# Performance work log

Measured on AMD Instinct MI355X. Metric: run time of the kernel, lower is better.

The kernel has to match this reference:

```python
import jax, jax.numpy as jnp
import numpy as np

N = 65536      # total nodes (64 graphs x 1024 nodes)
E = 1048576    # total edges
B = 64         # graphs in the batch
H = 128        # in_dim == hidden_dim
HEAD = 4
EPS = 1e-5


def setup_inputs() -> dict:
    key = jax.random.key(0)
    ks = jax.random.split(key, 16)
    s = 0.02
    return {
        "h": jax.random.normal(ks[0], (N, H), jnp.float32),
        "inter_f": jax.random.normal(ks[1], (B, H), jnp.float32),
        "gamma1": jnp.ones((H,), jnp.float32), "beta1": jnp.zeros((H,), jnp.float32),
        "W1": jax.random.normal(ks[2], (H, H), jnp.float32) * s, "b1": jnp.zeros((H,), jnp.float32),
        "gamma2": jnp.ones((H,), jnp.float32), "beta2": jnp.zeros((H,), jnp.float32),
        "W2": jax.random.normal(ks[3], (H, H), jnp.float32) * s, "b2": jnp.zeros((H,), jnp.float32),
        "Wq": jax.random.normal(ks[4], (HEAD, H, H), jnp.float32) * s,
        "Wk": jax.random.normal(ks[5], (HEAD, H, H), jnp.float32) * s,
        "Wv": jax.random.normal(ks[6], (HEAD, H, H), jnp.float32) * s,
        "Wc": jax.random.normal(ks[7], (HEAD * H, H), jnp.float32) * s,
        "ln_g": jnp.ones((H,), jnp.float32), "ln_b": jnp.zeros((H,), jnp.float32),
        "Wf1": jax.random.normal(ks[8], (H, 2 * H), jnp.float32) * s, "bf1": jnp.zeros((2 * H,), jnp.float32),
        "Wf2": jax.random.normal(ks[9], (2 * H, H), jnp.float32) * s, "bf2": jnp.zeros((H,), jnp.float32),
        "src": jax.random.randint(ks[10], (E,), 0, N, jnp.int32),
        "dst": jax.random.randint(ks[11], (E,), 0, N, jnp.int32),
        "graph_id": (jnp.arange(N) // (N // B)).astype(jnp.int32),
    }


def _bn(x, g, b):
    # BatchNorm1d (training-mode batch statistics, biased var)
    m = x.mean(0)
    v = jnp.mean((x - m) ** 2, 0)
    return (x - m) * jax.lax.rsqrt(v + EPS) * g + b


def _ln(x, g, b):
    m = x.mean(-1, keepdims=True)
    v = jnp.mean((x - m) ** 2, -1, keepdims=True)
    return (x - m) * jax.lax.rsqrt(v + EPS) * g + b


def _gconv(x, W, b, src, dst):
    # dgl GraphConv, norm='both': D_out^{-1/2} gather -> scatter-add -> D_in^{-1/2}, then W, b
    ones_e = jnp.ones((E,), x.dtype)
    dout = jnp.maximum(jax.ops.segment_sum(ones_e, src, num_segments=N), 1.0)
    din = jnp.maximum(jax.ops.segment_sum(ones_e, dst, num_segments=N), 1.0)
    msg = (x * jax.lax.rsqrt(dout)[:, None])[src]            # [E, H] gather
    agg = jax.ops.segment_sum(msg, dst, num_segments=N)      # [N, H] scatter-add
    agg = agg * jax.lax.rsqrt(din)[:, None]
    return agg @ W + b


def _forward(h, inter_f, gamma1, beta1, W1, b1, gamma2, beta2, W2, b2,
             Wq, Wk, Wv, Wc, ln_g, ln_b, Wf1, bf1, Wf2, bf2, src, dst, graph_id):
    # init pooling (mean_nodes)
    counts = jax.ops.segment_sum(jnp.ones((N,), h.dtype), graph_id, num_segments=B)
    init_avg_h = jax.ops.segment_sum(h, graph_id, num_segments=B) / counts[:, None]

    # two residual GraphConv blocks (dropout is identity at inference)
    h1 = h + jax.nn.relu(_gconv(_bn(h, gamma1, beta1), W1, b1, src, dst))
    h2 = h1 + jax.nn.relu(_gconv(_bn(h1, gamma2, beta2), W2, b2, src, dst))

    # broadcast_nodes(inter_f)
    inter_h = inter_f[graph_id]                               # [N, H]

    # transformer_block: per-head q/k/v, per-node scalar att, per-graph segment softmax
    q = jnp.einsum('nd,hdo->hno', h2, Wq)
    k = jnp.einsum('nd,hdo->hno', inter_h, Wk)
    v = jnp.einsum('nd,hdo->hno', h2, Wv)
    att = jnp.sum(q * k, axis=-1) / jnp.sqrt(jnp.float32(1280.0))   # [HEAD, N]
    mx = jax.vmap(lambda a: jax.ops.segment_max(a, graph_id, num_segments=B))(att)  # [HEAD, B]
    e = jnp.exp(att - mx[:, graph_id])
    ssum = jax.vmap(lambda a: jax.ops.segment_sum(a, graph_id, num_segments=B))(e)
    alpha = e / ssum[:, graph_id]                             # segment softmax per head
    tp = v * alpha[..., None]                                 # [HEAD, N, H]
    mo = tp.transpose(1, 0, 2).reshape(N, HEAD * H) @ Wc      # concat heads + project

    x1 = _ln(mo + h2, ln_g, ln_b)
    x2 = _ln(jax.nn.relu(x1 @ Wf1 + bf1) @ Wf2 + bf2 + x1, ln_g, ln_b)

    readout = jax.ops.segment_sum(x2, graph_id, num_segments=B)     # sum_nodes
    return readout, init_avg_h


def reference(h, inter_f, gamma1, beta1, W1, b1, gamma2, beta2, W2, b2,
              Wq, Wk, Wv, Wc, ln_g, ln_b, Wf1, bf1, Wf2, bf2, src, dst, graph_id):
    return _forward(h, inter_f, gamma1, beta1, W1, b1, gamma2, beta2, W2, b2,
                    Wq, Wk, Wv, Wc, ln_g, ln_b, Wf1, bf1, Wf2, bf2, src, dst, graph_id)
```

## Files before the change

kernel.cpp:

```cpp
#include <hip/hip_runtime.h>

#define NN 65536
#define NE 1048576
#define NB 64
#define HD 128
#define HD2 256
#define NHEAD 4
#define NPG 1024
#define BEPS 1e-5f
#define BM 64
#define ESTRIDE 20480

typedef short bf16x8s __attribute__((ext_vector_type(8)));
typedef float f32x4 __attribute__((ext_vector_type(4)));
#define MFMA16(a,b,c) __builtin_amdgcn_mfma_f32_16x16x32_bf16(a,b,c,0,0,0)

__device__ __forceinline__ unsigned short f2bf(float f) {
    union { float f; unsigned int u; } x{f};
    unsigned int r = x.u + 0x7FFFu + ((x.u >> 16) & 1u);
    return (unsigned short)(r >> 16);
}
__device__ __forceinline__ float b2f(unsigned short s) {
    union { unsigned int u; float f; } x{((unsigned int)s) << 16};
    return x.f;
}
__device__ __forceinline__ void atomAddF(float* p, float v) { unsafeAtomicAdd(p, v); }

__global__ __launch_bounds__(256) void k_prep_pool(const int* __restrict__ src, const int* __restrict__ dst,
                                                   int* __restrict__ gcurD, int* __restrict__ gcurS,
                                                   unsigned int* __restrict__ dbuck, unsigned short* __restrict__ sbuck,
                                                   const float* __restrict__ h, float* __restrict__ out_avg,
                                                   float* __restrict__ colsum, float* __restrict__ colsq) {
    __shared__ int cntD[64], cntS[64], baseD[64], baseS[64];
    __shared__ float ls[256], lq[256];
    const int t = threadIdx.x;
    if (blockIdx.x < 512) {
        if (t < 64) { cntD[t] = 0; cntS[t] = 0; }
        __syncthreads();
        const int e0 = blockIdx.x * 2048;
        int sv[8], dv[8];
        #pragma unroll
        for (int j = 0; j < 8; ++j) {
            int e = e0 + j * 256 + t;
            sv[j] = src[e]; dv[j] = dst[e];
            atomicAdd(&cntD[dv[j] >> 10], 1);
            atomicAdd(&cntS[sv[j] >> 10], 1);
        }
        __syncthreads();
        if (t < 64) baseD[t] = atomicAdd(&gcurD[t], cntD[t]);
        else if (t < 128) baseS[t - 64] = atomicAdd(&gcurS[t - 64], cntS[t - 64]);
        __syncthreads();
        if (t < 64) { cntD[t] = 0; cntS[t] = 0; }
        __syncthreads();
        #pragma unroll
        for (int j = 0; j < 8; ++j) {
            int gd = dv[j] >> 10;
            int slot = baseD[gd] + atomicAdd(&cntD[gd], 1);
            if (slot < ESTRIDE)
                dbuck[gd * ESTRIDE + slot] = (unsigned)(dv[j] & 1023) | ((unsigned)sv[j] << 10);
            int gs = sv[j] >> 10;
            int slot2 = baseS[gs] + atomicAdd(&cntS[gs], 1);
            if (slot2 < ESTRIDE)
                sbuck[gs * ESTRIDE + slot2] = (unsigned short)(sv[j] & 1023);
        }
    } else {
        int b2 = blockIdx.x - 512;
        int r0 = b2 * 64;
        int c = t & 127, half = t >> 7;
        float s = 0.f, sq = 0.f;
        for (int r = r0 + half * 32; r < r0 + half * 32 + 32; ++r) {
            float v = h[(size_t)r * HD + c];
            s += v; sq += v * v;
        }
        ls[t] = s; lq[t] = sq;
        __syncthreads();
        if (t < 128) {
            s = ls[t] + ls[t + 128]; sq = lq[t] + lq[t + 128];
            atomAddF(&out_avg[(r0 >> 10) * HD + t], s * (1.0f / NPG));
            atomAddF(&colsum[t], s);
            atomAddF(&colsq[t], sq);
        }
    }
}

__global__ __launch_bounds__(1024) void k_prep2(const int* __restrict__ gcurD, const int* __restrict__ gcurS,
                                                const unsigned int* __restrict__ dbuck,
                                                const unsigned short* __restrict__ sbuck,
                                                float* __restrict__ din_r, float* __restrict__ dout_r,
                                                int* __restrict__ beg, int* __restrict__ endv,
                                                int* __restrict__ elist) {
    __shared__ int hist[1024];
    __shared__ int pre[1024];
    const int t = threadIdx.x;
    const int b = blockIdx.x;
    if (b < 64) {
        const int g = b;
        const int n = min(gcurD[g], ESTRIDE);
        const unsigned int* pd = dbuck + g * ESTRIDE;
        hist[t] = 0;
        __syncthreads();
        for (int i = t; i < n; i += 1024) atomicAdd(&hist[pd[i] & 1023], 1);
        __syncthreads();
        const int cnt = hist[t];
        din_r[g * 1024 + t] = rsqrtf((float)max(cnt, 1));
        int x = cnt; pre[t] = x;
        __syncthreads();
        #pragma unroll
        for (int off = 1; off < 1024; off <<= 1) {
            int v = (t >= off) ? pre[t - off] : 0;
            __syncthreads();
            x += v; pre[t] = x;
            __syncthreads();
        }
        const int excl = x - cnt;
        beg[g * 1024 + t]  = g * ESTRIDE + excl;
        endv[g * 1024 + t] = g * ESTRIDE + excl + cnt;
        __syncthreads();
        hist[t] = excl; pre[t] = 0;
        __syncthreads();
        for (int i = t; i < n; i += 1024) {
            unsigned int w = pd[i];
            int dl = w & 1023;
            int r = atomicAdd(&pre[dl], 1);
            elist[g * ESTRIDE + hist[dl] + r] = (int)(w >> 10);
        }
    } else {
        const int g = b - 64;
        const int m = min(gcurS[g], ESTRIDE);
        const unsigned short* ps = sbuck + g * ESTRIDE;
        hist[t] = 0;
        __syncthreads();
        for (int i = t; i < m; i += 1024) atomicAdd(&hist[ps[i]], 1);
        __syncthreads();
        dout_r[g * 1024 + t] = rsqrtf((float)max(hist[t], 1));
    }
}

__device__ __forceinline__ void dev_prepW(int idx, const float* __restrict__ W,
                                          unsigned short* __restrict__ frag, int O) {
    int l = idx & 63, tt = idx >> 6;
    int ot = O >> 4;
    int c = tt % ot, ks = tt / ot;
    int q = l >> 4, m = l & 15;
    const float* wp = W + (size_t)(ks * 32 + q * 8) * O + c * 16 + m;
    union { uint4 v; unsigned short u[8]; } pk;
    #pragma unroll
    for (int j = 0; j < 8; ++j) pk.u[j] = f2bf(wp[(size_t)j * O]);
    *(uint4*)(frag + (size_t)idx * 8) = pk.v;
}

__global__ __launch_bounds__(256) void k_wprep(const float* __restrict__ W1, const float* __restrict__ W2,
                                               const float* __restrict__ Wf1, const float* __restrict__ Wf2,
                                               const float* __restrict__ interf, const float* __restrict__ Wk,
                                               const float* __restrict__ Wq, const float* __restrict__ Wv,
                                               const float* __restrict__ Wc,
                                               unsigned short* __restrict__ W1f, unsigned short* __restrict__ W2f,
                                               unsigned short* __restrict__ Wf1f, unsigned short* __restrict__ Wf2f,
                                               float* __restrict__ watt, unsigned short* __restrict__ Uf) {
    const int b = blockIdx.x, t = threadIdx.x;
    if (b < 8)        dev_prepW(b * 256 + t, W1, W1f, 128);
    else if (b < 16)  dev_prepW((b - 8) * 256 + t, W2, W2f, 128);
    else if (b < 32)  dev_prepW((b - 16) * 256 + t, Wf1, Wf1f, 256);
    else if (b < 48)  dev_prepW((b - 32) * 256 + t, Wf2, Wf2f, 128);
    else if (b < 304) {
        int hb = b - 48;
        int hh = hb >> 6, g = hb & 63;
        __shared__ float f[HD];
        __shared__ float kv[HD];
        if (t < HD) f[t] = interf[g * HD + t];
        __syncthreads();
        if (t < HD) {
            const float* Wkh = Wk + (size_t)hh * HD * HD;
            float s = 0.f;
            for (int d = 0; d < HD; ++d) s += f[d] * Wkh[(size_t)d * HD + t];
            kv[t] = s;
        }
        __syncthreads();
        if (t < HD) {
            const float* row = Wq + ((size_t)hh * HD + t) * HD;
            float s2 = 0.f;
            #pragma unroll 4
            for (int o = 0; o < HD; o += 4) {
                float4 w = *(const float4*)(row + o);
                s2 += w.x * kv[o] + w.y * kv[o + 1] + w.z * kv[o + 2] + w.w * kv[o + 3];
            }
            watt[hb * HD + t] = s2 * 0.027950849718747373f;
        }
    } else {
        int idx = (b - 304) * 256 + t;
        int o = idx & 127;
        int d = (idx >> 7) & 127;
        int hh = idx >> 14;
        const float* wv = Wv + ((size_t)hh * HD + d) * HD;
        const float* wc = Wc + (size_t)(hh * HD) * HD + o;
        float s = 0.f;
        for (int m2 = 0; m2 < HD; ++m2) s += wv[m2] * wc[(size_t)m2 * HD];
        int ks = d >> 5, dd = d & 31, q = dd >> 3, j = dd & 7;
        int c = o >> 4, m = o & 15, l = q * 16 + m;
        Uf[(size_t)((((hh * 4 + ks) * 8 + c) * 64 + l) * 8 + j)] = f2bf(s);
    }
}

__global__ __launch_bounds__(256) void k_bnpack(const float* __restrict__ x,
                                                const float* __restrict__ colsum, const float* __restrict__ colsq,
                                                const float* __restrict__ gma, const float* __restrict__ bta,
                                                const float* __restrict__ dout_r, unsigned short* __restrict__ xn) {
    int idx = blockIdx.x * 256 + threadIdx.x;
    int node = idx >> 4;
    int c8 = (idx & 15) * 8;
    float sc[8], sh[8];
    #pragma unroll
    for (int j = 0; j < 8; ++j) {
        float mean = colsum[c8 + j] * (1.0f / NN);
        float var  = colsq[c8 + j] * (1.0f / NN) - mean * mean;
        float rstd = rsqrtf(var + BEPS);
        sc[j] = rstd * gma[c8 + j];
        sh[j] = bta[c8 + j] - mean * sc[j];
    }
    float dr = dout_r[node];
    float4 v0 = *(const float4*)(x + (size_t)node * HD + c8);
    float4 v1 = *(const float4*)(x + (size_t)node * HD + c8 + 4);
    union { uint4 v; unsigned short u[8]; } pk;
    pk.u[0] = f2bf((v0.x * sc[0] + sh[0]) * dr);
    pk.u[1] = f2bf((v0.y * sc[1] + sh[1]) * dr);
    pk.u[2] = f2bf((v0.z * sc[2] + sh[2]) * dr);
    pk.u[3] = f2bf((v0.w * sc[3] + sh[3]) * dr);
    pk.u[4] = f2bf((v1.x * sc[4] + sh[4]) * dr);
    pk.u[5] = f2bf((v1.y * sc[5] + sh[5]) * dr);
    pk.u[6] = f2bf((v1.z * sc[6] + sh[6]) * dr);
    pk.u[7] = f2bf((v1.w * sc[7] + sh[7]) * dr);
    *(uint4*)(xn + (size_t)node * HD + c8) = pk.v;
}

__global__ __launch_bounds__(256) void k_aggregate(const unsigned short* __restrict__ xn,
                                                   const float* __restrict__ din_r,
                                                   const int* __restrict__ beg, const int* __restrict__ endv,
                                                   const int* __restrict__ elist,
                                                   unsigned short* __restrict__ agg) {
    const int tid = threadIdx.x;
    const int node = blockIdx.x * 4 + (tid >> 6);
    const int c2 = (tid & 63) * 2;
    const int b0 = beg[node], e0 = endv[node];
    float a0 = 0.f, a1 = 0.f;
    int i = b0;
    for (; i + 4 <= e0; i += 4) {
        int s0 = elist[i], s1 = elist[i + 1], s2 = elist[i + 2], s3 = elist[i + 3];
        unsigned int v0 = *(const unsigned int*)(xn + (size_t)s0 * HD + c2);
        unsigned int v1 = *(const unsigned int*)(xn + (size_t)s1 * HD + c2);
        unsigned int v2 = *(const unsigned int*)(xn + (size_t)s2 * HD + c2);
        unsigned int v3 = *(const unsigned int*)(xn + (size_t)s3 * HD + c2);
        a0 += b2f((unsigned short)v0) + b2f((unsigned short)v1) + b2f((unsigned short)v2) + b2f((unsigned short)v3);
        a1 += b2f((unsigned short)(v0 >> 16)) + b2f((unsigned short)(v1 >> 16))
            + b2f((unsigned short)(v2 >> 16)) + b2f((unsigned short)(v3 >> 16));
    }
    for (; i < e0; ++i) {
        int s = elist[i];
        unsigned int v = *(const unsigned int*)(xn + (size_t)s * HD + c2);
        a0 += b2f((unsigned short)v);
        a1 += b2f((unsigned short)(v >> 16));
    }
    float dn = din_r[node];
    ushort2 o;
    o.x = f2bf(a0 * dn); o.y = f2bf(a1 * dn);
    *(ushort2*)(agg + (size_t)node * HD + c2) = o;
}

template<bool SCORES, bool STATS>
__global__ __launch_bounds__(256) void k_gconv_mfma(const unsigned short* __restrict__ agg,
                                                    const unsigned short* __restrict__ Wfrag,
                                                    const float* __restrict__ bias,
                                                    const float* __restrict__ res, float* __restrict__ outp,
                                                    const float* __restrict__ watt, float* __restrict__ att,
                                                    float* __restrict__ colsum, float* __restrict__ colsq) {
    __shared__ float credS[4 * HD];
    __shared__ float credQ[4 * HD];
    const int tid = threadIdx.x;
    const int w = tid >> 6, l = tid & 63, q = l >> 4, m = l & 15;
    const int node = blockIdx.x * BM + w * 16 + m;
    bf16x8s a[4];
    #pragma unroll
    for (int ks = 0; ks < 4; ++ks)
        a[ks] = *(const bf16x8s*)(agg + (size_t)node * HD + ks * 32 + q * 8);
    f32x4 acc[8] = {};
    #pragma unroll
    for (int ks = 0; ks < 4; ++ks) {
        #pragma unroll
        for (int c = 0; c < 8; ++c) {
            bf16x8s b = *(const bf16x8s*)(Wfrag + (size_t)((ks * 8 + c) * 64 + l) * 8);
            acc[c] = MFMA16(b, a[ks], acc[c]);
        }
    }
    float vals[8][4];
    #pragma unroll
    for (int c = 0; c < 8; ++c) {
        const int col = c * 16 + q * 4;
        float4 bv = *(const float4*)(bias + col);
        float4 rv = *(const float4*)(res + (size_t)node * HD + col);
        vals[c][0] = rv.x + fmaxf(acc[c][0] + bv.x, 0.f);
        vals[c][1] = rv.y + fmaxf(acc[c][1] + bv.y, 0.f);
        vals[c][2] = rv.z + fmaxf(acc[c][2] + bv.z, 0.f);
        vals[c][3] = rv.w + fmaxf(acc[c][3] + bv.w, 0.f);
        *(float4*)(outp + (size_t)node * HD + col) = make_float4(vals[c][0], vals[c][1], vals[c][2], vals[c][3]);
    }
    if (SCORES) {
        const int g = node >> 10;
        #pragma unroll
        for (int hh = 0; hh < NHEAD; ++hh) {
            const float* wp = watt + ((size_t)(hh * NB + g)) * HD;
            float s = 0.f;
            #pragma unroll
            for (int c = 0; c < 8; ++c) {
                const int col = c * 16 + q * 4;
                float4 wv = *(const float4*)(wp + col);
                s += vals[c][0] * wv.x + vals[c][1] * wv.y + vals[c][2] * wv.z + vals[c][3] * wv.w;
            }
            s += __shfl_xor(s, 16, 64);
            s += __shfl_xor(s, 32, 64);
            if (q == 0) att[(size_t)hh * NN + node] = s;
        }
    }
    if (STATS) {
        #pragma unroll
        for (int c = 0; c < 8; ++c) {
            #pragma unroll
            for (int r = 0; r < 4; ++r) {
                float v = vals[c][r];
                float vq = v * v;
                #pragma unroll
                for (int mk = 1; mk <= 8; mk <<= 1) {
                    v  += __shfl_xor(v, mk, 64);
                    vq += __shfl_xor(vq, mk, 64);
                }
                if (m == 0) {
                    credS[w * HD + c * 16 + q * 4 + r] = v;
                    credQ[w * HD + c * 16 + q * 4 + r] = vq;
                }
            }
        }
        __syncthreads();
        if (tid < HD) {
            float s = credS[tid] + credS[HD + tid] + credS[2 * HD + tid] + credS[3 * HD + tid];
            float sq = credQ[tid] + credQ[HD + tid] + credQ[2 * HD + tid] + credQ[3 * HD + tid];
            atomAddF(&colsum[tid], s);
            atomAddF(&colsq[tid], sq);
        }
    }
}

__global__ __launch_bounds__(256) void k_segsoftmax(const float* __restrict__ att, float* __restrict__ alpha) {
    const int hh = blockIdx.x >> 6, g = blockIdx.x & 63;
    const int t = threadIdx.x;
    const float* a = att + (size_t)hh * NN + g * NPG;
    float* al = alpha + (size_t)hh * NN + g * NPG;
    float v[4]; float mx = -1e30f;
    #pragma unroll
    for (int i = 0; i < 4; ++i) { v[i] = a[t + i * 256]; mx = fmaxf(mx, v[i]); }
    #pragma unroll
    for (int m = 32; m > 0; m >>= 1) mx = fmaxf(mx, __shfl_xor(mx, m, 64));
    __shared__ float redm[4], reds[4];
    if ((t & 63) == 0) redm[t >> 6] = mx;
    __syncthreads();
    mx = fmaxf(fmaxf(redm[0], redm[1]), fmaxf(redm[2], redm[3]));
    float s = 0.f;
    #pragma unroll
    for (int i = 0; i < 4; ++i) { v[i] = __expf(v[i] - mx); s += v[i]; }
    #pragma unroll
    for (int m = 32; m > 0; m >>= 1) s += __shfl_xor(s, m, 64);
    if ((t & 63) == 0) reds[t >> 6] = s;
    __syncthreads();
    s = reds[0] + reds[1] + reds[2] + reds[3];
    float inv = 1.f / s;
    #pragma unroll
    for (int i = 0; i < 4; ++i) al[t + i * 256] = v[i] * inv;
}

__global__ __launch_bounds__(256) void k_mo_x1(const float* __restrict__ h2,
                                               const unsigned short* __restrict__ Ufrag,
                                               const float* __restrict__ alpha,
                                               const float* __restrict__ lng, const float* __restrict__ lnb,
                                               float* __restrict__ x1) {
    const int tid = threadIdx.x;
    const int w = tid >> 6, l = tid & 63, q = l >> 4, m = l & 15;
    const int node = blockIdx.x * BM + w * 16 + m;
    bf16x8s a[4];
    #pragma unroll
    for (int ks = 0; ks < 4; ++ks) {
        float4 v0 = *(const float4*)(h2 + (size_t)node * HD + ks * 32 + q * 8);
        float4 v1 = *(const float4*)(h2 + (size_t)node * HD + ks * 32 + q * 8 + 4);
        union { bf16x8s v; unsigned short u[8]; } pk;
        pk.u[0] = f2bf(v0.x); pk.u[1] = f2bf(v0.y); pk.u[2] = f2bf(v0.z); pk.u[3] = f2bf(v0.w);
        pk.u[4] = f2bf(v1.x); pk.u[5] = f2bf(v1.y); pk.u[6] = f2bf(v1.z); pk.u[7] = f2bf(v1.w);
        a[ks] = pk.v;
    }
    f32x4 mo[8] = {};
    #pragma unroll
    for (int hh = 0; hh < 4; ++hh) {
        f32x4 acc[8] = {};
        #pragma unroll
        for (int ks = 0; ks < 4; ++ks) {
            #pragma unroll
            for (int c = 0; c < 8; ++c) {
                bf16x8s b = *(const bf16x8s*)(Ufrag + (size_t)(((hh * 4 + ks) * 8 + c) * 64 + l) * 8);
                acc[c] = MFMA16(b, a[ks], acc[c]);
            }
        }
        float al = alpha[(size_t)hh * NN + node];
        #pragma unroll
        for (int c = 0; c < 8; ++c) {
            mo[c][0] += al * acc[c][0];
            mo[c][1] += al * acc[c][1];
            mo[c][2] += al * acc[c][2];
            mo[c][3] += al * acc[c][3];
        }
    }
    float vals[8][4]; float s = 0.f, sq = 0.f;
    #pragma unroll
    for (int c = 0; c < 8; ++c) {
        const int col = c * 16 + q * 4;
        float4 hv = *(const float4*)(h2 + (size_t)node * HD + col);
        vals[c][0] = mo[c][0] + hv.x;
        vals[c][1] = mo[c][1] + hv.y;
        vals[c][2] = mo[c][2] + hv.z;
        vals[c][3] = mo[c][3] + hv.w;
        #pragma unroll
        for (int r = 0; r < 4; ++r) { s += vals[c][r]; sq += vals[c][r] * vals[c][r]; }
    }
    s  += __shfl_xor(s, 16, 64);  s  += __shfl_xor(s, 32, 64);
    sq += __shfl_xor(sq, 16, 64); sq += __shfl_xor(sq, 32, 64);
    float mean = s * (1.f / HD);
    float var  = sq * (1.f / HD) - mean * mean;
    float rstd = rsqrtf(var + BEPS);
    #pragma unroll
    for (int c = 0; c < 8; ++c) {
        const int col = c * 16 + q * 4;
        float4 gv = *(const float4*)(lng + col);
        float4 bv = *(const float4*)(lnb + col);
        float4 o;
        o.x = (vals[c][0] - mean) * rstd * gv.x + bv.x;
        o.y = (vals[c][1] - mean) * rstd * gv.y + bv.y;
        o.z = (vals[c][2] - mean) * rstd * gv.z + bv.z;
        o.w = (vals[c][3] - mean) * rstd * gv.w + bv.w;
        *(float4*)(x1 + (size_t)node * HD + col) = o;
    }
}

__global__ __launch_bounds__(256) void k_ffn1_mfma(const float* __restrict__ X,
                                                   const unsigned short* __restrict__ Wfrag,
                                                   const float* __restrict__ bias,
                                                   unsigned short* __restrict__ mid) {
    const int tid = threadIdx.x;
    const int w = tid >> 6, l = tid & 63, q = l >> 4, m = l & 15;
    const int node = blockIdx.x * BM + w * 16 + m;
    bf16x8s a[4];
    #pragma unroll
    for (int ks = 0; ks < 4; ++ks) {
        float4 v0 = *(const float4*)(X + (size_t)node * HD + ks * 32 + q * 8);
        float4 v1 = *(const float4*)(X + (size_t)node * HD + ks * 32 + q * 8 + 4);
        union { bf16x8s v; unsigned short u[8]; } pk;
        pk.u[0] = f2bf(v0.x); pk.u[1] = f2bf(v0.y); pk.u[2] = f2bf(v0.z); pk.u[3] = f2bf(v0.w);
        pk.u[4] = f2bf(v1.x); pk.u[5] = f2bf(v1.y); pk.u[6] = f2bf(v1.z); pk.u[7] = f2bf(v1.w);
        a[ks] = pk.v;
    }
    f32x4 acc[16] = {};
    #pragma unroll
    for (int ks = 0; ks < 4; ++ks) {
        #pragma unroll
        for (int c = 0; c < 16; ++c) {
            bf16x8s b = *(const bf16x8s*)(Wfrag + (size_t)((ks * 16 + c) * 64 + l) * 8);
            acc[c] = MFMA16(b, a[ks], acc[c]);
        }
    }
    #pragma unroll
    for (int c = 0; c < 16; ++c) {
        const int col = c * 16 + q * 4;
        float4 bv = *(const float4*)(bias + col);
        ushort4 o;
        o.x = f2bf(fmaxf(acc[c][0] + bv.x, 0.f));
        o.y = f2bf(fmaxf(acc[c][1] + bv.y, 0.f));
        o.z = f2bf(fmaxf(acc[c][2] + bv.z, 0.f));
        o.w = f2bf(fmaxf(acc[c][3] + bv.w, 0.f));
        *(ushort4*)(mid + (size_t)node * HD2 + col) = o;
    }
}

__global__ __launch_bounds__(256) void k_ffn2_mfma(const unsigned short* __restrict__ mid,
                                                   const unsigned short* __restrict__ Wfrag,
                                                   const float* __restrict__ bias,
                                                   const float* __restrict__ x1,
                                                   const float* __restrict__ lng, const float* __restrict__ lnb,
                                                   float* __restrict__ outp) {
    __shared__ float cred[4 * HD];
    const int tid = threadIdx.x;
    const int w = tid >> 6, l = tid & 63, q = l >> 4, m = l & 15;
    const int node = blockIdx.x * BM + w * 16 + m;
    bf16x8s a[8];
    #pragma unroll
    for (int ks = 0; ks < 8; ++ks)
        a[ks] = *(const bf16x8s*)(mid + (size_t)node * HD2 + ks * 32 + q * 8);
    f32x4 acc[8] = {};
    #pragma unroll
    for (int ks = 0; ks < 8; ++ks) {
        #pragma unroll
        for (int c = 0; c < 8; ++c) {
            bf16x8s b = *(const bf16x8s*)(Wfrag + (size_t)((ks * 8 + c) * 64 + l) * 8);
            acc[c] = MFMA16(b, a[ks], acc[c]);
        }
    }
    float vals[8][4]; float s = 0.f, sq = 0.f;
    #pragma unroll
    for (int c = 0; c < 8; ++c) {
        const int col = c * 16 + q * 4;
        float4 bv = *(const float4*)(bias + col);
        float4 xv = *(const float4*)(x1 + (size_t)node * HD + col);
        vals[c][0] = acc[c][0] + bv.x + xv.x;
        vals[c][1] = acc[c][1] + bv.y + xv.y;
        vals[c][2] = acc[c][2] + bv.z + xv.z;
        vals[c][3] = acc[c][3] + bv.w + xv.w;
        #pragma unroll
        for (int r = 0; r < 4; ++r) { s += vals[c][r]; sq += vals[c][r] * vals[c][r]; }
    }
    s  += __shfl_xor(s, 16, 64);  s  += __shfl_xor(s, 32, 64);
    sq += __shfl_xor(sq, 16, 64); sq += __shfl_xor(sq, 32, 64);
    float mean = s * (1.f / HD);
    float var  = sq * (1.f / HD) - mean * mean;
    float rstd = rsqrtf(var + BEPS);
    #pragma unroll
    for (int c = 0; c < 8; ++c) {
        const int col = c * 16 + q * 4;
        float4 gv = *(const float4*)(lng + col);
        float4 bv = *(const float4*)(lnb + col);
        float4 o;
        o.x = (vals[c][0] - mean) * rstd * gv.x + bv.x;
        o.y = (vals[c][1] - mean) * rstd * gv.y + bv.y;
        o.z = (vals[c][2] - mean) * rstd * gv.z + bv.z;
        o.w = (vals[c][3] - mean) * rstd * gv.w + bv.w;
        #pragma unroll
        for (int mk = 1; mk <= 8; mk <<= 1) {
            o.x += __shfl_xor(o.x, mk, 64);
            o.y += __shfl_xor(o.y, mk, 64);
            o.z += __shfl_xor(o.z, mk, 64);
            o.w += __shfl_xor(o.w, mk, 64);
        }
        if (m == 0) *(float4*)(cred + w * HD + col) = o;
    }
    __syncthreads();
    if (tid < HD) {
        float sum = cred[tid] + cred[HD + tid] + cred[2 * HD + tid] + cred[3 * HD + tid];
        int g = blockIdx.x >> 4;
        atomAddF(&outp[g * HD + tid], sum);
    }
}

extern "C" void kernel_launch(void* const* d_in, const int* in_sizes, int n_in,
                              void* d_out, int out_size, void* d_ws, size_t ws_size,
                              hipStream_t stream) {
    (void)in_sizes; (void)n_in; (void)out_size;
    const float* h      = (const float*)d_in[0];
    const float* interf = (const float*)d_in[1];
    const float* gamma1 = (const float*)d_in[2];
    const float* beta1  = (const float*)d_in[3];
    const float* W1     = (const float*)d_in[4];
    const float* b1     = (const float*)d_in[5];
    const float* gamma2 = (const float*)d_in[6];
    const float* beta2  = (const float*)d_in[7];
    const float* W2     = (const float*)d_in[8];
    const float* b2     = (const float*)d_in[9];
    const float* Wq     = (const float*)d_in[10];
    const float* Wk     = (const float*)d_in[11];
    const float* Wv     = (const float*)d_in[12];
    const float* Wc     = (const float*)d_in[13];
    const float* ln_g   = (const float*)d_in[14];
    const float* ln_b   = (const float*)d_in[15];
    const float* Wf1    = (const float*)d_in[16];
    const float* bf1    = (const float*)d_in[17];
    const float* Wf2    = (const float*)d_in[18];
    const float* bf2    = (const float*)d_in[19];
    const int*   src    = (const int*)d_in[20];
    const int*   dst    = (const int*)d_in[21];

    float* out = (float*)d_out;
    float* R1 = (float*)d_ws;
    float* R2 = R1 + 8388608;
    float* R3 = R2 + 8388608;
    float* aux = R3 + 8388608;

    float* h1 = R1;
    float* x1 = R1;
    unsigned int*   dbuck = (unsigned int*)R1;
    unsigned short* sbuck = (unsigned short*)(R1 + 1310720);
    float* h2 = R2;
    int*   elist = (int*)R2;
    unsigned short* mid  = (unsigned short*)R2;
    unsigned short* xn   = (unsigned short*)R3;
    unsigned short* aggb = (unsigned short*)(R3 + 4194304);
    float* att   = R3;
    float* alpha = R3 + 262144;

    float* dout_r  = aux;
    float* din_r   = aux + 65536;
    float* colsum1 = aux + 131072;
    float* colsq1  = aux + 131200;
    float* colsum2 = aux + 131328;
    float* colsq2  = aux + 131456;
    int*   gcurD   = (int*)(aux + 131584);
    int*   gcurS   = (int*)(aux + 131648);
    float* watt    = aux + 131712;
    int*   beg     = (int*)(aux + 164480);
    int*   endv    = (int*)(aux + 230016);
    unsigned short* W1f  = (unsigned short*)(aux + 295552);
    unsigned short* W2f  = (unsigned short*)(aux + 303744);
    unsigned short* Wf1f = (unsigned short*)(aux + 311936);
    unsigned short* Wf2f = (unsigned short*)(aux + 328320);
    unsigned short* Uf   = (unsigned short*)(aux + 344704);

    if (ws_size < (size_t)(25165824 + 377472) * 4) return;

    hipMemsetAsync(out, 0, 16384 * 4, stream);
    hipMemsetAsync(colsum1, 0, 640 * 4, stream);

    k_prep_pool<<<1536, 256, 0, stream>>>(src, dst, gcurD, gcurS, dbuck, sbuck,
                                          h, out + 8192, colsum1, colsq1);
    k_prep2<<<128, 1024, 0, stream>>>(gcurD, gcurS, dbuck, sbuck, din_r, dout_r, beg, endv, elist);
    k_wprep<<<560, 256, 0, stream>>>(W1, W2, Wf1, Wf2, interf, Wk, Wq, Wv, Wc,
                                     W1f, W2f, Wf1f, Wf2f, watt, Uf);

    k_bnpack<<<4096, 256, 0, stream>>>(h, colsum1, colsq1, gamma1, beta1, dout_r, xn);
    k_aggregate<<<16384, 256, 0, stream>>>(xn, din_r, beg, endv, elist, aggb);
    k_gconv_mfma<false, true><<<1024, 256, 0, stream>>>(aggb, W1f, b1, h, h1, nullptr, nullptr, colsum2, colsq2);

    k_bnpack<<<4096, 256, 0, stream>>>(h1, colsum2, colsq2, gamma2, beta2, dout_r, xn);
    k_aggregate<<<16384, 256, 0, stream>>>(xn, din_r, beg, endv, elist, aggb);
    k_gconv_mfma<true, false><<<1024, 256, 0, stream>>>(aggb, W2f, b2, h1, h2, watt, att, nullptr, nullptr);

    k_segsoftmax<<<256, 256, 0, stream>>>(att, alpha);
    k_mo_x1<<<1024, 256, 0, stream>>>(h2, Uf, alpha, ln_g, ln_b, x1);

    k_ffn1_mfma<<<1024, 256, 0, stream>>>(x1, Wf1f, bf1, mid);
    k_ffn2_mfma<<<1024, 256, 0, stream>>>(mid, Wf2f, bf2, x1, ln_g, ln_b, out);
}
```

Before: 339.6 us.

## Fuse attention, FFN and readout into one kernel; bf16 intermediates; deterministic reductions

Merges the multi-head attention projection, the first LayerNorm, both FFN matmuls and the second LayerNorm into one kernel that keeps x1 and the FFN hidden activations in shared memory instead of round-tripping them through global memory. The h1 and h2 intermediates are now stored as bf16 instead of fp32, which halves their traffic but adds rounding error to residuals and BN statistics. Float atomics for column statistics and the readout are replaced by per-block partial buffers plus small reduction kernels, and the edge-bucketing kernel moves to larger blocks with padded global counters. These steps add kernel launches and change numerical precision in exchange for less memory traffic and less atomic contention.

```diff
diff --git a/kernel.cpp b/kernel.cpp
--- a/kernel.cpp
+++ b/kernel.cpp
@@ -24,36 +24,34 @@
     union { unsigned int u; float f; } x{((unsigned int)s) << 16};
     return x.f;
 }
-__device__ __forceinline__ void atomAddF(float* p, float v) { unsafeAtomicAdd(p, v); }
-
-__global__ __launch_bounds__(256) void k_prep_pool(const int* __restrict__ src, const int* __restrict__ dst,
-                                                   int* __restrict__ gcurD, int* __restrict__ gcurS,
-                                                   unsigned int* __restrict__ dbuck, unsigned short* __restrict__ sbuck,
-                                                   const float* __restrict__ h, float* __restrict__ out_avg,
-                                                   float* __restrict__ colsum, float* __restrict__ colsq) {
-    __shared__ int cntD[64], cntS[64], baseD[64], baseS[64];
-    __shared__ float ls[256], lq[256];
+
+__global__ __launch_bounds__(1024) void k_prep_pool(const int* __restrict__ src, const int* __restrict__ dst,
+                                                    int* __restrict__ gcurD, int* __restrict__ gcurS,
+                                                    unsigned int* __restrict__ dbuck, unsigned short* __restrict__ sbuck,
+                                                    const float* __restrict__ h,
+                                                    float* __restrict__ psum, float* __restrict__ psq) {
     const int t = threadIdx.x;
-    if (blockIdx.x < 512) {
+    if (blockIdx.x < 64) {
+        __shared__ int cntD[64], cntS[64], baseD[64], baseS[64];
         if (t < 64) { cntD[t] = 0; cntS[t] = 0; }
         __syncthreads();
-        const int e0 = blockIdx.x * 2048;
-        int sv[8], dv[8];
-        #pragma unroll
-        for (int j = 0; j < 8; ++j) {
-            int e = e0 + j * 256 + t;
+        const int e0 = blockIdx.x * 16384;
+        int sv[16], dv[16];
+        #pragma unroll
+        for (int j = 0; j < 16; ++j) {
+            int e = e0 + j * 1024 + t;
             sv[j] = src[e]; dv[j] = dst[e];
             atomicAdd(&cntD[dv[j] >> 10], 1);
             atomicAdd(&cntS[sv[j] >> 10], 1);
         }
         __syncthreads();
-        if (t < 64) baseD[t] = atomicAdd(&gcurD[t], cntD[t]);
-        else if (t < 128) baseS[t - 64] = atomicAdd(&gcurS[t - 64], cntS[t - 64]);
+        if (t < 64) baseD[t] = atomicAdd(&gcurD[t * 32], cntD[t]);
+        else if (t < 128) baseS[t - 64] = atomicAdd(&gcurS[(t - 64) * 32], cntS[t - 64]);
         __syncthreads();
         if (t < 64) { cntD[t] = 0; cntS[t] = 0; }
         __syncthreads();
         #pragma unroll
-        for (int j = 0; j < 8; ++j) {
+        for (int j = 0; j < 16; ++j) {
             int gd = dv[j] >> 10;
             int slot = baseD[gd] + atomicAdd(&cntD[gd], 1);
             if (slot < ESTRIDE)
@@ -64,21 +62,23 @@
                 sbuck[gs * ESTRIDE + slot2] = (unsigned short)(sv[j] & 1023);
         }
     } else {
-        int b2 = blockIdx.x - 512;
-        int r0 = b2 * 64;
-        int c = t & 127, half = t >> 7;
+        __shared__ float ls[1024], lq[1024];
+        const int bb = blockIdx.x - 64;
+        const int r0 = bb * 256;
+        const int c = t & 127, strip8 = t >> 7;
         float s = 0.f, sq = 0.f;
-        for (int r = r0 + half * 32; r < r0 + half * 32 + 32; ++r) {
-            float v = h[(size_t)r * HD + c];
+        for (int i = 0; i < 32; ++i) {
+            float v = h[(size_t)(r0 + strip8 * 32 + i) * HD + c];
             s += v; sq += v * v;
         }
         ls[t] = s; lq[t] = sq;
         __syncthreads();
         if (t < 128) {
-            s = ls[t] + ls[t + 128]; sq = lq[t] + lq[t + 128];
-            atomAddF(&out_avg[(r0 >> 10) * HD + t], s * (1.0f / NPG));
-            atomAddF(&colsum[t], s);
-            atomAddF(&colsq[t], sq);
+            float ss = 0.f, qq = 0.f;
+            #pragma unroll
+            for (int k = 0; k < 8; ++k) { ss += ls[t + k * 128]; qq += lq[t + k * 128]; }
+            psum[bb * HD + t] = ss;
+            psq[bb * HD + t]  = qq;
         }
     }
 }
@@ -95,7 +95,7 @@
     const int b = blockIdx.x;
     if (b < 64) {
         const int g = b;
-        const int n = min(gcurD[g], ESTRIDE);
+        const int n = min(gcurD[g * 32], ESTRIDE);
         const unsigned int* pd = dbuck + g * ESTRIDE;
         hist[t] = 0;
         __syncthreads();
@@ -126,7 +126,7 @@
         }
     } else {
         const int g = b - 64;
-        const int m = min(gcurS[g], ESTRIDE);
+        const int m = min(gcurS[g * 32], ESTRIDE);
         const unsigned short* ps = sbuck + g * ESTRIDE;
         hist[t] = 0;
         __syncthreads();
@@ -156,7 +156,10 @@
                                                const float* __restrict__ Wc,
                                                unsigned short* __restrict__ W1f, unsigned short* __restrict__ W2f,
                                                unsigned short* __restrict__ Wf1f, unsigned short* __restrict__ Wf2f,
-                                               float* __restrict__ watt, unsigned short* __restrict__ Uf) {
+                                               float* __restrict__ watt, unsigned short* __restrict__ Uf,
+                                               const float* __restrict__ psum, const float* __restrict__ psq,
+                                               float* __restrict__ out_avg,
+                                               float* __restrict__ colsum, float* __restrict__ colsq) {
     const int b = blockIdx.x, t = threadIdx.x;
     if (b < 8)        dev_prepW(b * 256 + t, W1, W1f, 128);
     else if (b < 16)  dev_prepW((b - 8) * 256 + t, W2, W2f, 128);
@@ -186,7 +189,7 @@
             }
             watt[hb * HD + t] = s2 * 0.027950849718747373f;
         }
-    } else {
+    } else if (b < 560) {
         int idx = (b - 304) * 256 + t;
         int o = idx & 127;
         int d = (idx >> 7) & 127;
@@ -198,10 +201,29 @@
         int ks = d >> 5, dd = d & 31, q = dd >> 3, j = dd & 7;
         int c = o >> 4, m = o & 15, l = q * 16 + m;
         Uf[(size_t)((((hh * 4 + ks) * 8 + c) * 64 + l) * 8 + j)] = f2bf(s);
-    }
-}
-
-__global__ __launch_bounds__(256) void k_bnpack(const float* __restrict__ x,
+    } else {
+        const int col = b - 560;
+        __shared__ float ls[256], lq[256];
+        ls[t] = psum[t * HD + col];
+        lq[t] = psq[t * HD + col];
+        __syncthreads();
+        if (t < 64) {
+            float a4 = ls[4 * t] + ls[4 * t + 1] + ls[4 * t + 2] + ls[4 * t + 3];
+            out_avg[t * HD + col] = a4 * (1.0f / NPG);
+            float b4 = lq[4 * t] + lq[4 * t + 1] + lq[4 * t + 2] + lq[4 * t + 3];
+            float ts = a4, tq = b4;
+            #pragma unroll
+            for (int mk = 1; mk <= 32; mk <<= 1) {
+                ts += __shfl_xor(ts, mk, 64);
+                tq += __shfl_xor(tq, mk, 64);
+            }
+            if (t == 0) { colsum[col] = ts; colsq[col] = tq; }
+        }
+    }
+}
+
+template<bool IN32>
+__global__ __launch_bounds__(256) void k_bnpack(const void* __restrict__ xin,
                                                 const float* __restrict__ colsum, const float* __restrict__ colsq,
                                                 const float* __restrict__ gma, const float* __restrict__ bta,
                                                 const float* __restrict__ dout_r, unsigned short* __restrict__ xn) {
@@ -218,17 +240,23 @@
         sh[j] = bta[c8 + j] - mean * sc[j];
     }
     float dr = dout_r[node];
-    float4 v0 = *(const float4*)(x + (size_t)node * HD + c8);
-    float4 v1 = *(const float4*)(x + (size_t)node * HD + c8 + 4);
+    float v[8];
+    if (IN32) {
+        const float* x = (const float*)xin;
+        float4 v0 = *(const float4*)(x + (size_t)node * HD + c8);
+        float4 v1 = *(const float4*)(x + (size_t)node * HD + c8 + 4);
+        v[0] = v0.x; v[1] = v0.y; v[2] = v0.z; v[3] = v0.w;
+        v[4] = v1.x; v[5] = v1.y; v[6] = v1.z; v[7] = v1.w;
+    } else {
+        const unsigned short* x = (const unsigned short*)xin;
+        union { uint4 u; unsigned short s[8]; } r;
+        r.u = *(const uint4*)(x + (size_t)node * HD + c8);
+        #pragma unroll
+        for (int j = 0; j < 8; ++j) v[j] = b2f(r.s[j]);
+    }
     union { uint4 v; unsigned short u[8]; } pk;
-    pk.u[0] = f2bf((v0.x * sc[0] + sh[0]) * dr);
-    pk.u[1] = f2bf((v0.y * sc[1] + sh[1]) * dr);
-    pk.u[2] = f2bf((v0.z * sc[2] + sh[2]) * dr);
-    pk.u[3] = f2bf((v0.w * sc[3] + sh[3]) * dr);
-    pk.u[4] = f2bf((v1.x * sc[4] + sh[4]) * dr);
-    pk.u[5] = f2bf((v1.y * sc[5] + sh[5]) * dr);
-    pk.u[6] = f2bf((v1.z * sc[6] + sh[6]) * dr);
-    pk.u[7] = f2bf((v1.w * sc[7] + sh[7]) * dr);
+    #pragma unroll
+    for (int j = 0; j < 8; ++j) pk.u[j] = f2bf((v[j] * sc[j] + sh[j]) * dr);
     *(uint4*)(xn + (size_t)node * HD + c8) = pk.v;
 }
 
@@ -265,13 +293,13 @@
     *(ushort2*)(agg + (size_t)node * HD + c2) = o;
 }
 
-template<bool SCORES, bool STATS>
+template<bool SCORES, bool STATS, bool RES32>
 __global__ __launch_bounds__(256) void k_gconv_mfma(const unsigned short* __restrict__ agg,
                                                     const unsigned short* __restrict__ Wfrag,
                                                     const float* __restrict__ bias,
-                                                    const float* __restrict__ res, float* __restrict__ outp,
+                                                    const void* __restrict__ res, unsigned short* __restrict__ outp,
                                                     const float* __restrict__ watt, float* __restrict__ att,
-                                                    float* __restrict__ colsum, float* __restrict__ colsq) {
+                                                    float* __restrict__ part2s, float* __restrict__ part2q) {
     __shared__ float credS[4 * HD];
     __shared__ float credQ[4 * HD];
     const int tid = threadIdx.x;
@@ -295,12 +323,22 @@
     for (int c = 0; c < 8; ++c) {
         const int col = c * 16 + q * 4;
         float4 bv = *(const float4*)(bias + col);
-        float4 rv = *(const float4*)(res + (size_t)node * HD + col);
-        vals[c][0] = rv.x + fmaxf(acc[c][0] + bv.x, 0.f);
-        vals[c][1] = rv.y + fmaxf(acc[c][1] + bv.y, 0.f);
-        vals[c][2] = rv.z + fmaxf(acc[c][2] + bv.z, 0.f);
-        vals[c][3] = rv.w + fmaxf(acc[c][3] + bv.w, 0.f);
-        *(float4*)(outp + (size_t)node * HD + col) = make_float4(vals[c][0], vals[c][1], vals[c][2], vals[c][3]);
+        float rv[4];
+        if (RES32) {
+            float4 r4 = *(const float4*)((const float*)res + (size_t)node * HD + col);
+            rv[0] = r4.x; rv[1] = r4.y; rv[2] = r4.z; rv[3] = r4.w;
+        } else {
+            ushort4 r4 = *(const ushort4*)((const unsigned short*)res + (size_t)node * HD + col);
+            rv[0] = b2f(r4.x); rv[1] = b2f(r4.y); rv[2] = b2f(r4.z); rv[3] = b2f(r4.w);
+        }
+        vals[c][0] = rv[0] + fmaxf(acc[c][0] + bv.x, 0.f);
+        vals[c][1] = rv[1] + fmaxf(acc[c][1] + bv.y, 0.f);
+        vals[c][2] = rv[2] + fmaxf(acc[c][2] + bv.z, 0.f);
+        vals[c][3] = rv[3] + fmaxf(acc[c][3] + bv.w, 0.f);
+        ushort4 o;
+        o.x = f2bf(vals[c][0]); o.y = f2bf(vals[c][1]);
+        o.z = f2bf(vals[c][2]); o.w = f2bf(vals[c][3]);
+        *(ushort4*)(outp + (size_t)node * HD + col) = o;
     }
     if (SCORES) {
         const int g = node >> 10;
@@ -339,12 +377,33 @@
         }
         __syncthreads();
         if (tid < HD) {
-            float s = credS[tid] + credS[HD + tid] + credS[2 * HD + tid] + credS[3 * HD + tid];
-            float sq = credQ[tid] + credQ[HD + tid] + credQ[2 * HD + tid] + credQ[3 * HD + tid];
-            atomAddF(&colsum[tid], s);
-            atomAddF(&colsq[tid], sq);
-        }
-    }
+            part2s[(size_t)blockIdx.x * HD + tid] =
+                credS[tid] + credS[HD + tid] + credS[2 * HD + tid] + credS[3 * HD + tid];
+            part2q[(size_t)blockIdx.x * HD + tid] =
+                credQ[tid] + credQ[HD + tid] + credQ[2 * HD + tid] + credQ[3 * HD + tid];
+        }
+    }
+}
+
+__global__ __launch_bounds__(256) void k_red2(const float* __restrict__ part2s, const float* __restrict__ part2q,
+                                              float* __restrict__ colsum, float* __restrict__ colsq) {
+    __shared__ float ws[8];
+    const int col = blockIdx.x, t = threadIdx.x;
+    float s = 0.f, sq = 0.f;
+    #pragma unroll
+    for (int k = 0; k < 4; ++k) {
+        s  += part2s[(size_t)(t + k * 256) * HD + col];
+        sq += part2q[(size_t)(t + k * 256) * HD + col];
+    }
+    #pragma unroll
+    for (int mk = 1; mk <= 32; mk <<= 1) {
+        s  += __shfl_xor(s, mk, 64);
+        sq += __shfl_xor(sq, mk, 64);
+    }
+    if ((t & 63) == 0) { ws[(t >> 6) * 2] = s; ws[(t >> 6) * 2 + 1] = sq; }
+    __syncthreads();
+    if (t == 0) colsum[col] = ws[0] + ws[2] + ws[4] + ws[6];
+    if (t == 1) colsq[col]  = ws[1] + ws[3] + ws[5] + ws[7];
 }
 
 __global__ __launch_bounds__(256) void k_segsoftmax(const float* __restrict__ att, float* __restrict__ alpha) {
@@ -374,24 +433,26 @@
     for (int i = 0; i < 4; ++i) al[t + i * 256] = v[i] * inv;
 }
 
-__global__ __launch_bounds__(256) void k_mo_x1(const float* __restrict__ h2,
-                                               const unsigned short* __restrict__ Ufrag,
-                                               const float* __restrict__ alpha,
-                                               const float* __restrict__ lng, const float* __restrict__ lnb,
-                                               float* __restrict__ x1) {
+__global__ __launch_bounds__(256) void k_mega(const unsigned short* __restrict__ h2b,
+                                              const unsigned short* __restrict__ Ufrag,
+                                              const float* __restrict__ alpha,
+                                              const float* __restrict__ lng, const float* __restrict__ lnb,
+                                              const unsigned short* __restrict__ Wf1f,
+                                              const unsigned short* __restrict__ Wf2f,
+                                              const float* __restrict__ bf1v, const float* __restrict__ bf2v,
+                                              float* __restrict__ rpart) {
+    __shared__ unsigned short x1l[64][136];
+    __shared__ unsigned short midl[64][264];
+    __shared__ float cred[4 * HD];
     const int tid = threadIdx.x;
     const int w = tid >> 6, l = tid & 63, q = l >> 4, m = l & 15;
     const int node = blockIdx.x * BM + w * 16 + m;
+    const int row = w * 16 + m;
+
     bf16x8s a[4];
     #pragma unroll
-    for (int ks = 0; ks < 4; ++ks) {
-        float4 v0 = *(const float4*)(h2 + (size_t)node * HD + ks * 32 + q * 8);
-        float4 v1 = *(const float4*)(h2 + (size_t)node * HD + ks * 32 + q * 8 + 4);
-        union { bf16x8s v; unsigned short u[8]; } pk;
-        pk.u[0] = f2bf(v0.x); pk.u[1] = f2bf(v0.y); pk.u[2] = f2bf(v0.z); pk.u[3] = f2bf(v0.w);
-        pk.u[4] = f2bf(v1.x); pk.u[5] = f2bf(v1.y); pk.u[6] = f2bf(v1.z); pk.u[7] = f2bf(v1.w);
-        a[ks] = pk.v;
-    }
+    for (int ks = 0; ks < 4; ++ks)
+        a[ks] = *(const bf16x8s*)(h2b + (size_t)node * HD + ks * 32 + q * 8);
     f32x4 mo[8] = {};
     #pragma unroll
     for (int hh = 0; hh < 4; ++hh) {
@@ -413,15 +474,90 @@
             mo[c][3] += al * acc[c][3];
         }
     }
+    {
+        float vals[8][4]; float s = 0.f, sq = 0.f;
+        #pragma unroll
+        for (int c = 0; c < 8; ++c) {
+            const int col = c * 16 + q * 4;
+            ushort4 hv = *(const ushort4*)(h2b + (size_t)node * HD + col);
+            vals[c][0] = mo[c][0] + b2f(hv.x);
+            vals[c][1] = mo[c][1] + b2f(hv.y);
+            vals[c][2] = mo[c][2] + b2f(hv.z);
+            vals[c][3] = mo[c][3] + b2f(hv.w);
+            #pragma unroll
+            for (int r = 0; r < 4; ++r) { s += vals[c][r]; sq += vals[c][r] * vals[c][r]; }
+        }
+        s  += __shfl_xor(s, 16, 64);  s  += __shfl_xor(s, 32, 64);
+        sq += __shfl_xor(sq, 16, 64); sq += __shfl_xor(sq, 32, 64);
+        float mean = s * (1.f / HD);
+        float var  = sq * (1.f / HD) - mean * mean;
+        float rstd = rsqrtf(var + BEPS);
+        #pragma unroll
+        for (int c = 0; c < 8; ++c) {
+            const int col = c * 16 + q * 4;
+            float4 gv = *(const float4*)(lng + col);
+            float4 bv = *(const float4*)(lnb + col);
+            ushort4 o;
+            o.x = f2bf((vals[c][0] - mean) * rstd * gv.x + bv.x);
+            o.y = f2bf((vals[c][1] - mean) * rstd * gv.y + bv.y);
+            o.z = f2bf((vals[c][2] - mean) * rstd * gv.z + bv.z);
+            o.w = f2bf((vals[c][3] - mean) * rstd * gv.w + bv.w);
+            *(ushort4*)(&x1l[row][col]) = o;
+        }
+    }
+    __syncthreads();
+
+    {
+        bf16x8s a2[4];
+        #pragma unroll
+        for (int ks = 0; ks < 4; ++ks)
+            a2[ks] = *(const bf16x8s*)(&x1l[row][ks * 32 + q * 8]);
+        f32x4 accB[16] = {};
+        #pragma unroll
+        for (int ks = 0; ks < 4; ++ks) {
+            #pragma unroll
+            for (int c = 0; c < 16; ++c) {
+                bf16x8s b = *(const bf16x8s*)(Wf1f + (size_t)((ks * 16 + c) * 64 + l) * 8);
+                accB[c] = MFMA16(b, a2[ks], accB[c]);
+            }
+        }
+        #pragma unroll
+        for (int c = 0; c < 16; ++c) {
+            const int col = c * 16 + q * 4;
+            float4 bv = *(const float4*)(bf1v + col);
+            ushort4 o;
+            o.x = f2bf(fmaxf(accB[c][0] + bv.x, 0.f));
+            o.y = f2bf(fmaxf(accB[c][1] + bv.y, 0.f));
+            o.z = f2bf(fmaxf(accB[c][2] + bv.z, 0.f));
+            o.w = f2bf(fmaxf(accB[c][3] + bv.w, 0.f));
+            *(ushort4*)(&midl[row][col]) = o;
+        }
+    }
+    __syncthreads();
+
+    bf16x8s a3[8];
+    #pragma unroll
+    for (int ks = 0; ks < 8; ++ks)
+        a3[ks] = *(const bf16x8s*)(&midl[row][ks * 32 + q * 8]);
+    f32x4 accC[8] = {};
+    #pragma unroll
+    for (int ks = 0; ks < 8; ++ks) {
+        #pragma unroll
+        for (int c = 0; c < 8; ++c) {
+            bf16x8s b = *(const bf16x8s*)(Wf2f + (size_t)((ks * 8 + c) * 64 + l) * 8);
+            accC[c] = MFMA16(b, a3[ks], accC[c]);
+        }
+    }
     float vals[8][4]; float s = 0.f, sq = 0.f;
     #pragma unroll
     for (int c = 0; c < 8; ++c) {
         const int col = c * 16 + q * 4;
-        float4 hv = *(const float4*)(h2 + (size_t)node * HD + col);
-        vals[c][0] = mo[c][0] + hv.x;
-        vals[c][1] = mo[c][1] + hv.y;
-        vals[c][2] = mo[c][2] + hv.z;
-        vals[c][3] = mo[c][3] + hv.w;
+        float4 bv = *(const float4*)(bf2v + col);
+        ushort4 xv = *(const ushort4*)(&x1l[row][col]);
+        vals[c][0] = accC[c][0] + bv.x + b2f(xv.x);
+        vals[c][1] = accC[c][1] + bv.y + b2f(xv.y);
+        vals[c][2] = accC[c][2] + bv.z + b2f(xv.z);
+        vals[c][3] = accC[c][3] + bv.w + b2f(xv.w);
         #pragma unroll
         for (int r = 0; r < 4; ++r) { s += vals[c][r]; sq += vals[c][r] * vals[c][r]; }
     }
@@ -440,100 +576,6 @@
         o.y = (vals[c][1] - mean) * rstd * gv.y + bv.y;
         o.z = (vals[c][2] - mean) * rstd * gv.z + bv.z;
         o.w = (vals[c][3] - mean) * rstd * gv.w + bv.w;
-        *(float4*)(x1 + (size_t)node * HD + col) = o;
-    }
-}
-
-__global__ __launch_bounds__(256) void k_ffn1_mfma(const float* __restrict__ X,
-                                                   const unsigned short* __restrict__ Wfrag,
-                                                   const float* __restrict__ bias,
-                                                   unsigned short* __restrict__ mid) {
-    const int tid = threadIdx.x;
-    const int w = tid >> 6, l = tid & 63, q = l >> 4, m = l & 15;
-    const int node = blockIdx.x * BM + w * 16 + m;
-    bf16x8s a[4];
-    #pragma unroll
-    for (int ks = 0; ks < 4; ++ks) {
-        float4 v0 = *(const float4*)(X + (size_t)node * HD + ks * 32 + q * 8);
-        float4 v1 = *(const float4*)(X + (size_t)node * HD + ks * 32 + q * 8 + 4);
-        union { bf16x8s v; unsigned short u[8]; } pk;
-        pk.u[0] = f2bf(v0.x); pk.u[1] = f2bf(v0.y); pk.u[2] = f2bf(v0.z); pk.u[3] = f2bf(v0.w);
-        pk.u[4] = f2bf(v1.x); pk.u[5] = f2bf(v1.y); pk.u[6] = f2bf(v1.z); pk.u[7] = f2bf(v1.w);
-        a[ks] = pk.v;
-    }
-    f32x4 acc[16] = {};
-    #pragma unroll
-    for (int ks = 0; ks < 4; ++ks) {
-        #pragma unroll
-        for (int c = 0; c < 16; ++c) {
-            bf16x8s b = *(const bf16x8s*)(Wfrag + (size_t)((ks * 16 + c) * 64 + l) * 8);
-            acc[c] = MFMA16(b, a[ks], acc[c]);
-        }
-    }
-    #pragma unroll
-    for (int c = 0; c < 16; ++c) {
-        const int col = c * 16 + q * 4;
-        float4 bv = *(const float4*)(bias + col);
-        ushort4 o;
-        o.x = f2bf(fmaxf(acc[c][0] + bv.x, 0.f));
-        o.y = f2bf(fmaxf(acc[c][1] + bv.y, 0.f));
-        o.z = f2bf(fmaxf(acc[c][2] + bv.z, 0.f));
-        o.w = f2bf(fmaxf(acc[c][3] + bv.w, 0.f));
-        *(ushort4*)(mid + (size_t)node * HD2 + col) = o;
-    }
-}
-
-__global__ __launch_bounds__(256) void k_ffn2_mfma(const unsigned short* __restrict__ mid,
-                                                   const unsigned short* __restrict__ Wfrag,
-                                                   const float* __restrict__ bias,
-                                                   const float* __restrict__ x1,
-                                                   const float* __restrict__ lng, const float* __restrict__ lnb,
-                                                   float* __restrict__ outp) {
-    __shared__ float cred[4 * HD];
-    const int tid = threadIdx.x;
-    const int w = tid >> 6, l = tid & 63, q = l >> 4, m = l & 15;
-    const int node = blockIdx.x * BM + w * 16 + m;
-    bf16x8s a[8];
-    #pragma unroll
-    for (int ks = 0; ks < 8; ++ks)
-        a[ks] = *(const bf16x8s*)(mid + (size_t)node * HD2 + ks * 32 + q * 8);
-    f32x4 acc[8] = {};
-    #pragma unroll
-    for (int ks = 0; ks < 8; ++ks) {
-        #pragma unroll
-        for (int c = 0; c < 8; ++c) {
-            bf16x8s b = *(const bf16x8s*)(Wfrag + (size_t)((ks * 8 + c) * 64 + l) * 8);
-            acc[c] = MFMA16(b, a[ks], acc[c]);
-        }
-    }
-    float vals[8][4]; float s = 0.f, sq = 0.f;
-    #pragma unroll
-    for (int c = 0; c < 8; ++c) {
-        const int col = c * 16 + q * 4;
-        float4 bv = *(const float4*)(bias + col);
-        float4 xv = *(const float4*)(x1 + (size_t)node * HD + col);
-        vals[c][0] = acc[c][0] + bv.x + xv.x;
-        vals[c][1] = acc[c][1] + bv.y + xv.y;
-        vals[c][2] = acc[c][2] + bv.z + xv.z;
-        vals[c][3] = acc[c][3] + bv.w + xv.w;
-        #pragma unroll
-        for (int r = 0; r < 4; ++r) { s += vals[c][r]; sq += vals[c][r] * vals[c][r]; }
-    }
-    s  += __shfl_xor(s, 16, 64);  s  += __shfl_xor(s, 32, 64);
-    sq += __shfl_xor(sq, 16, 64); sq += __shfl_xor(sq, 32, 64);
-    float mean = s * (1.f / HD);
-    float var  = sq * (1.f / HD) - mean * mean;
-    float rstd = rsqrtf(var + BEPS);
-    #pragma unroll
-    for (int c = 0; c < 8; ++c) {
-        const int col = c * 16 + q * 4;
-        float4 gv = *(const float4*)(lng + col);
-        float4 bv = *(const float4*)(lnb + col);
-        float4 o;
-        o.x = (vals[c][0] - mean) * rstd * gv.x + bv.x;
-        o.y = (vals[c][1] - mean) * rstd * gv.y + bv.y;
-        o.z = (vals[c][2] - mean) * rstd * gv.z + bv.z;
-        o.w = (vals[c][3] - mean) * rstd * gv.w + bv.w;
         #pragma unroll
         for (int mk = 1; mk <= 8; mk <<= 1) {
             o.x += __shfl_xor(o.x, mk, 64);
@@ -544,11 +586,22 @@
         if (m == 0) *(float4*)(cred + w * HD + col) = o;
     }
     __syncthreads();
-    if (tid < HD) {
-        float sum = cred[tid] + cred[HD + tid] + cred[2 * HD + tid] + cred[3 * HD + tid];
-        int g = blockIdx.x >> 4;
-        atomAddF(&outp[g * HD + tid], sum);
-    }
+    if (tid < HD)
+        rpart[(size_t)blockIdx.x * HD + tid] =
+            cred[tid] + cred[HD + tid] + cred[2 * HD + tid] + cred[3 * HD + tid];
+}
+
+__global__ __launch_bounds__(256) void k_redout(const float* __restrict__ rpart, float* __restrict__ outp) {
+    __shared__ float ls[256];
+    const int g = blockIdx.x, t = threadIdx.x;
+    const int c = t & 127, half = t >> 7;
+    float s = 0.f;
+    #pragma unroll
+    for (int k = 0; k < 8; ++k)
+        s += rpart[(size_t)(g * 16 + half * 8 + k) * HD + c];
+    ls[t] = s;
+    __syncthreads();
+    if (t < 128) outp[g * HD + t] = ls[t] + ls[t + 128];
 }
 
 extern "C" void kernel_launch(void* const* d_in, const int* in_sizes, int n_in,
@@ -584,17 +637,20 @@
     float* R3 = R2 + 8388608;
     float* aux = R3 + 8388608;
 
-    float* h1 = R1;
-    float* x1 = R1;
     unsigned int*   dbuck = (unsigned int*)R1;
     unsigned short* sbuck = (unsigned short*)(R1 + 1310720);
-    float* h2 = R2;
+    unsigned short* h1b   = (unsigned short*)R1;
     int*   elist = (int*)R2;
-    unsigned short* mid  = (unsigned short*)R2;
+    unsigned short* h2b   = (unsigned short*)R2;
+    float* psum  = R2 + 4194304;
+    float* psq   = R2 + 4227072;
     unsigned short* xn   = (unsigned short*)R3;
     unsigned short* aggb = (unsigned short*)(R3 + 4194304);
-    float* att   = R3;
-    float* alpha = R3 + 262144;
+    float* att    = R3;
+    float* alpha  = R3 + 262144;
+    float* part2s = R3 + 2097152;
+    float* part2q = R3 + 2228224;
+    float* rpart  = R3 + 4194304;
 
     float* dout_r  = aux;
     float* din_r   = aux + 65536;
@@ -603,38 +659,38 @@
     float* colsum2 = aux + 131328;
     float* colsq2  = aux + 131456;
     int*   gcurD   = (int*)(aux + 131584);
-    int*   gcurS   = (int*)(aux + 131648);
-    float* watt    = aux + 131712;
-    int*   beg     = (int*)(aux + 164480);
-    int*   endv    = (int*)(aux + 230016);
-    unsigned short* W1f  = (unsigned short*)(aux + 295552);
-    unsigned short* W2f  = (unsigned short*)(aux + 303744);
-    unsigned short* Wf1f = (unsigned short*)(aux + 311936);
-    unsigned short* Wf2f = (unsigned short*)(aux + 328320);
-    unsigned short* Uf   = (unsigned short*)(aux + 344704);
-
-    if (ws_size < (size_t)(25165824 + 377472) * 4) return;
-
-    hipMemsetAsync(out, 0, 16384 * 4, stream);
-    hipMemsetAsync(colsum1, 0, 640 * 4, stream);
-
-    k_prep_pool<<<1536, 256, 0, stream>>>(src, dst, gcurD, gcurS, dbuck, sbuck,
-                                          h, out + 8192, colsum1, colsq1);
+    int*   gcurS   = (int*)(aux + 133632);
+    float* watt    = aux + 135680;
+    int*   beg     = (int*)(aux + 168448);
+    int*   endv    = (int*)(aux + 233984);
+    unsigned short* W1f  = (unsigned short*)(aux + 299520);
+    unsigned short* W2f  = (unsigned short*)(aux + 307712);
+    unsigned short* Wf1f = (unsigned short*)(aux + 315904);
+    unsigned short* Wf2f = (unsigned short*)(aux + 332288);
+    unsigned short* Uf   = (unsigned short*)(aux + 348672);
+
+    if (ws_size < (size_t)(25165824 + 381440) * 4) return;
+
+    hipMemsetAsync(gcurD, 0, 4096 * sizeof(int), stream);
+
+    k_prep_pool<<<320, 1024, 0, stream>>>(src, dst, gcurD, gcurS, dbuck, sbuck, h, psum, psq);
     k_prep2<<<128, 1024, 0, stream>>>(gcurD, gcurS, dbuck, sbuck, din_r, dout_r, beg, endv, elist);
-    k_wprep<<<560, 256, 0, stream>>>(W1, W2, Wf1, Wf2, interf, Wk, Wq, Wv, Wc,
-                                     W1f, W2f, Wf1f, Wf2f, watt, Uf);
-
-    k_bnpack<<<4096, 256, 0, stream>>>(h, colsum1, colsq1, gamma1, beta1, dout_r, xn);
+    k_wprep<<<688, 256, 0, stream>>>(W1, W2, Wf1, Wf2, interf, Wk, Wq, Wv, Wc,
+                                     W1f, W2f, Wf1f, Wf2f, watt, Uf,
+                                     psum, psq, out + 8192, colsum1, colsq1);
+
+    k_bnpack<true><<<4096, 256, 0, stream>>>(h, colsum1, colsq1, gamma1, beta1, dout_r, xn);
     k_aggregate<<<16384, 256, 0, stream>>>(xn, din_r, beg, endv, elist, aggb);
-    k_gconv_mfma<false, true><<<1024, 256, 0, stream>>>(aggb, W1f, b1, h, h1, nullptr, nullptr, colsum2, colsq2);
-
-    k_bnpack<<<4096, 256, 0, stream>>>(h1, colsum2, colsq2, gamma2, beta2, dout_r, xn);
+    k_gconv_mfma<false, true, true><<<1024, 256, 0, stream>>>(aggb, W1f, b1, h, h1b,
+                                                              nullptr, nullptr, part2s, part2q);
+    k_red2<<<128, 256, 0, stream>>>(part2s, part2q, colsum2, colsq2);
+
+    k_bnpack<false><<<4096, 256, 0, stream>>>(h1b, colsum2, colsq2, gamma2, beta2, dout_r, xn);
     k_aggregate<<<16384, 256, 0, stream>>>(xn, din_r, beg, endv, elist, aggb);
-    k_gconv_mfma<true, false><<<1024, 256, 0, stream>>>(aggb, W2f, b2, h1, h2, watt, att, nullptr, nullptr);
+    k_gconv_mfma<true, false, false><<<1024, 256, 0, stream>>>(aggb, W2f, b2, h1b, h2b,
+                                                               watt, att, nullptr, nullptr);
 
     k_segsoftmax<<<256, 256, 0, stream>>>(att, alpha);
-    k_mo_x1<<<1024, 256, 0, stream>>>(h2, Uf, alpha, ln_g, ln_b, x1);
-
-    k_ffn1_mfma<<<1024, 256, 0, stream>>>(x1, Wf1f, bf1, mid);
-    k_ffn2_mfma<<<1024, 256, 0, stream>>>(mid, Wf2f, bf2, x1, ln_g, ln_b, out);
-}
+    k_mega<<<1024, 256, 0, stream>>>(h2b, Uf, alpha, ln_g, ln_b, Wf1f, Wf2f, bf1, bf2, rpart);
+    k_redout<<<64, 256, 0, stream>>>(rpart, out);
+}
```

New measurement: 381.2 us. 1.12x slower.
